# Performance work log

Measured on AMD Instinct MI355X. Metric: run time of the kernel, lower is better.

## Reference

```python
import jax, jax.numpy as jnp
import numpy as np

GAMMA = 2.0
ALPHA_CLASS = 0.01
ALPHA_COORD = 1.0

def _xywh_to_xyxy(b):
    # [.., 4] (x, y, w, h) -> (x1, y1, x2, y2)
    return jnp.concatenate([b[..., :2], b[..., :2] + b[..., 2:]], axis=-1)

def _jaccard(a, b):
    # a: [A,4] xyxy, b: [N,4] xyxy -> IoU [A,N]
    lt = jnp.maximum(a[:, None, :2], b[None, :, :2])
    rb = jnp.minimum(a[:, None, 2:], b[None, :, 2:])
    wh = jnp.clip(rb - lt, 0.0)
    inter = wh[..., 0] * wh[..., 1]
    area_a = (a[:, 2] - a[:, 0]) * (a[:, 3] - a[:, 1])
    area_b = (b[:, 2] - b[:, 0]) * (b[:, 3] - b[:, 1])
    return inter / (area_a[:, None] + area_b[None, :] - inter)

def _match_mask(thr, anchors, gt_xywh, num_obj):
    # Returns positive (anchor, gt) pair mask [A, N_max], honoring gt[:num_obj].
    A = anchors.shape[0]
    N = gt_xywh.shape[0]
    gt_boxes = _xywh_to_xyxy(gt_xywh)
    ious = _jaccard(anchors, gt_boxes)              # [A, N]
    valid = jnp.arange(N) < num_obj                 # [N]
    ious_v = jnp.where(valid[None, :], ious, -jnp.inf)
    best_gt_idx = jnp.argmax(ious_v, axis=0)        # [N] best anchor per gt
    forced = jnp.arange(A)[:, None] == best_gt_idx[None, :]  # positive_mask[best,i]=1
    return ((ious > thr) | forced) & valid[None, :]

def _class_loss_item(thr, classes, anchors, gt, num_obj):
    # classes: [A,2] probs (col0 = background, col1 = face)
    mask = _match_mask(thr, anchors, gt, num_obj)   # [A, N]
    counts = jnp.sum(mask, axis=1)                  # [A] multiplicity of each anchor in positive_idx
    is_pos = counts > 0                             # dedup, as index_fill_ does
    probs = jnp.where(is_pos, classes[:, 1], classes[:, 0])
    focal = -((1.0 - probs) ** GAMMA) * jnp.log(probs)
    # extra = focal_loss.index_select(0, positive_idx) keeps duplicates -> weight by counts
    extra = jnp.sum(counts.astype(focal.dtype) * focal)
    return jnp.sum(focal) + 10.0 * extra

def setup_inputs() -> dict:
    key = jax.random.key(0)
    B, A, N = 16, 131072, 64
    k1, k2, k3, k4, k5, k6 = jax.random.split(key, 6)
    # anchors in xyxy, valid boxes in [0,1]
    a_xy = jax.random.uniform(k1, (A, 2), jnp.float32, 0.0, 0.8)
    a_wh = jax.random.uniform(k2, (A, 2), jnp.float32, 0.05, 0.2)
    anchors = jnp.concatenate([a_xy, a_xy + a_wh], axis=-1)
    # class probabilities strictly in (0,1) for log()
    batch_classes = jax.random.uniform(k3, (B, A, 2), jnp.float32, 0.05, 0.95)
    g_xy = jax.random.uniform(k4, (B, N, 2), jnp.float32, 0.0, 0.8)
    g_wh = jax.random.uniform(k5, (B, N, 2), jnp.float32, 0.05, 0.2)
    batch_gt = jnp.concatenate([g_xy, g_wh], axis=-1)  # xywh
    batch_num_objects = jax.random.randint(k6, (B,), 1, N + 1, jnp.int32)
    return {
        "threshhold": jnp.float32(0.5),
        "batch_classes": batch_classes,
        "anchors": anchors,
        "batch_gt": batch_gt,
        "batch_num_objects": batch_num_objects,
    }

def reference(threshhold, batch_classes, anchors, batch_gt, batch_num_objects):
    R = batch_classes.shape[0]
    per_item = jax.vmap(lambda c, g, n: _class_loss_item(threshhold, c, anchors, g, n))
    class_loss = jnp.sum(per_item(batch_classes, batch_gt, batch_num_objects))
    class_loss = class_loss * ALPHA_CLASS / R
    # Faithful to the source: coord_loss is initialized to zero and never accumulated
    coord_loss = jnp.zeros((), batch_classes.dtype) * ALPHA_COORD / R
    total_loss = class_loss + coord_loss
    return (total_loss, class_loss, coord_loss)
```

## Files before the change

kernel.cpp:

```cpp
#include <hip/hip_runtime.h>

#define NANCH   131072
#define NMAX    64
#define NBATCH  16
#define THREADS 256
#define APT     4
#define ACH     (THREADS * APT)
#define NCHUNK  (NANCH / ACH)
#define NPAIR   (NBATCH / 2)
#define NBLK    (NCHUNK * NPAIR)
#define GTG     8


__global__ __launch_bounds__(64) void k_setup(
    const int* __restrict__ nobj, unsigned long long* __restrict__ cells,
    int* __restrict__ pairs)
{
    int tid = threadIdx.x;
    for (int i = tid; i < NBATCH * NMAX; i += 64) cells[i] = 0ull;
    if (tid == 0) {
        int idx[NBATCH], key[NBATCH];
        for (int i = 0; i < NBATCH; ++i) { idx[i] = i; key[i] = nobj[i]; }
        for (int i = 1; i < NBATCH; ++i) {
            int kj = key[i], ij = idx[i], j = i - 1;
            while (j >= 0 && key[j] < kj) { key[j+1]=key[j]; idx[j+1]=idx[j]; --j; }
            key[j+1] = kj; idx[j+1] = ij;
        }
        for (int p = 0; p < NPAIR; ++p) {
            pairs[2*p]   = idx[p];
            pairs[2*p+1] = idx[NBATCH-1-p];
        }
    }
}

__global__ __launch_bounds__(THREADS) void k_phase(
    const float* __restrict__ thr_p,
    const float* __restrict__ classes,
    const float* __restrict__ anchors,
    const float* __restrict__ gt,
    const int*   __restrict__ nobj,
    const int*   __restrict__ pairs,
    unsigned long long* __restrict__ cells,
    double* __restrict__ partials)
{
    int chunk = blockIdx.x / NPAIR;
    int pr    = blockIdx.x % NPAIR;
    int tid   = threadIdx.x;
    float thr = *thr_p;
    float t1  = 1.0f + thr;
    int b0 = pairs[2*pr], b1 = pairs[2*pr+1];

    __shared__ float4 sbox[2*NMAX];
    __shared__ float  sgar[2*NMAX];
    __shared__ float  stsg[2*NMAX];
    __shared__ int    sno[2];
    __shared__ unsigned long long spk[4][GTG];
    __shared__ double sw[4];

    for (int j = tid; j < 2*NMAX; j += THREADS) {
        int s = j >> 6, n = j & 63;
        int b = s ? b1 : b0;
        int no = nobj[b];
        float4 g = reinterpret_cast<const float4*>(gt)[b*NMAX + n];
        float x2 = g.x + g.z, y2 = g.y + g.w;
        float4 box = make_float4(g.x, g.y, x2, y2);
        float  ar  = (x2 - g.x) * (y2 - g.y);
        if (n >= no) { box = make_float4(4.f,4.f,4.f,4.f); ar = 0.f; }
        sbox[j] = box; sgar[j] = ar; stsg[j] = thr * ar;
    }
    if (tid < 2) sno[tid] = nobj[tid ? b1 : b0];
    __syncthreads();

    float ax1[APT], ay1[APT], ax2[APT], ay2[APT], aar[APT], ta[APT];
    int abase = chunk * ACH + tid;
    #pragma unroll
    for (int k = 0; k < APT; ++k) {
        float4 v = reinterpret_cast<const float4*>(anchors)[abase + k*THREADS];
        ax1[k]=v.x; ay1[k]=v.y; ax2[k]=v.z; ay2[k]=v.w;
        aar[k] = (v.z - v.x) * (v.w - v.y);
        ta[k]  = thr * aar[k];
    }

    int wv = tid >> 6, ln = tid & 63;
    double acc = 0.0;

    for (int s = 0; s < 2; ++s) {
        int b    = s ? b1 : b0;
        int no   = sno[s];
        int base = s * NMAX;
        int cnt[APT] = {0,0,0,0};

        for (int g0 = 0; g0 < no; g0 += GTG) {
            float bn[GTG], bd[GTG]; int bx[GTG];
            #pragma unroll
            for (int n = 0; n < GTG; ++n) { bn[n] = -1.f; bd[n] = 1.f; bx[n] = 0; }

            #pragma unroll
            for (int n = 0; n < GTG; ++n) {
                float4 g  = sbox[base + g0 + n];
                float gar = sgar[base + g0 + n];
                float tsg = stsg[base + g0 + n];
                #pragma unroll
                for (int k = 0; k < APT; ++k) {
                    float lx = fmaxf(ax1[k], g.x);
                    float ly = fmaxf(ay1[k], g.y);
                    float rx = fminf(ax2[k], g.z);
                    float ry = fminf(ay2[k], g.w);
                    float w  = fmaxf(rx - lx, 0.f);
                    float h  = fmaxf(ry - ly, 0.f);
                    float inter = w * h;
                    float den   = (aar[k] + gar) - inter;
                    cnt[k] += (inter * t1 > ta[k] + tsg) ? 1 : 0;
                    bool better = inter * bd[n] > bn[n] * den;
                    bn[n] = better ? inter : bn[n];
                    bd[n] = better ? den   : bd[n];
                    bx[n] = better ? (abase + k*THREADS) : bx[n];
                }
            }

            unsigned long long pk[GTG];
            #pragma unroll
            for (int n = 0; n < GTG; ++n) {
                float iou = bn[n] * __builtin_amdgcn_rcpf(bd[n]);
                pk[n] = ((unsigned long long)__float_as_uint(iou) << 32)
                      | (unsigned long long)(0x7FFFFFFFu - (unsigned)bx[n]);
            }
            #pragma unroll
            for (int off = 32; off; off >>= 1) {
                #pragma unroll
                for (int n = 0; n < GTG; ++n) {
                    unsigned long long o = __shfl_xor(pk[n], off, 64);
                    if (o > pk[n]) pk[n] = o;
                }
            }
            if (ln == 0) {
                #pragma unroll
                for (int n = 0; n < GTG; ++n) spk[wv][n] = pk[n];
            }
            __syncthreads();
            if (tid < GTG && g0 + tid < no) {
                unsigned long long m0 = spk[0][tid] > spk[1][tid] ? spk[0][tid] : spk[1][tid];
                unsigned long long m1 = spk[2][tid] > spk[3][tid] ? spk[2][tid] : spk[3][tid];
                unsigned long long m  = m0 > m1 ? m0 : m1;
                atomicMax(&cells[b*NMAX + g0 + tid], m);
            }
            __syncthreads();
        }

        const float2* cp = reinterpret_cast<const float2*>(classes) + (size_t)b * NANCH;
        #pragma unroll
        for (int k = 0; k < APT; ++k) {
            float2 c = cp[abase + k*THREADS];
            float p  = (cnt[k] > 0) ? c.y : c.x;
            float om = 1.0f - p;
            float focal = -om * om * __logf(p);
            acc += (double)(focal * (1.0f + 10.0f * (float)cnt[k]));
        }
    }

    #pragma unroll
    for (int off = 32; off; off >>= 1) acc += __shfl_xor(acc, off, 64);
    if (ln == 0) sw[wv] = acc;
    __syncthreads();
    if (tid == 0) partials[blockIdx.x] = sw[0] + sw[1] + sw[2] + sw[3];
}

__global__ __launch_bounds__(1024) void k_tail(
    const float* __restrict__ thr_p,
    const float* __restrict__ classes,
    const float* __restrict__ anchors,
    const float* __restrict__ gt,
    const int*   __restrict__ nobj,
    const unsigned long long* __restrict__ cells,
    const double* __restrict__ partials,
    float* __restrict__ out)
{
    int tid = threadIdx.x;
    int b = tid >> 6, n = tid & 63;
    float thr = *thr_p;
    float t1  = 1.0f + thr;

    __shared__ float4 sbox[NBATCH*NMAX];
    __shared__ float  stsa[NBATCH*NMAX];
    __shared__ int    sidx[NBATCH*NMAX];
    __shared__ double sdelta[NBATCH];
    __shared__ double sw[16];

    int n_obj = nobj[b];
    {
        float4 g = reinterpret_cast<const float4*>(gt)[b*NMAX + n];
        float x2 = g.x + g.z, y2 = g.y + g.w;
        sbox[tid] = make_float4(g.x, g.y, x2, y2);
        stsa[tid] = thr * ((x2 - g.x) * (y2 - g.y));
    }
    __syncthreads();

    int bi = -1; bool need = false;
    float4 av = make_float4(0.f,0.f,0.f,0.f);
    float ta = 0.f;
    if (n < n_obj) {
        unsigned long long pkv = cells[tid];
        bi = (int)(0x7FFFFFFFu - (unsigned)(pkv & 0xFFFFFFFFull));
        av = reinterpret_cast<const float4*>(anchors)[bi];
        float aar = (av.z - av.x) * (av.w - av.y);
        ta = thr * aar;
        float4 g = sbox[tid];
        float lx = fmaxf(av.x, g.x), ly = fmaxf(av.y, g.y);
        float rx = fminf(av.z, g.z), ry = fminf(av.w, g.w);
        float w  = fmaxf(rx - lx, 0.f), h = fmaxf(ry - ly, 0.f);
        float inter = w * h;
        need = !(inter * t1 > ta + stsa[tid]);
    }
    sidx[tid] = need ? bi : -1;
    __syncthreads();

    double delta = 0.0;
    if (need) {
        bool first = true; int extra = 0;
        int base = b * NMAX;
        for (int m = 0; m < NMAX; ++m) {
            if (sidx[base + m] == bi) { if (m < n) first = false; ++extra; }
        }
        if (first) {
            int count = 0;
            for (int m = 0; m < n_obj; ++m) {
                float4 g = sbox[base + m];
                float lx = fmaxf(av.x, g.x), ly = fmaxf(av.y, g.y);
                float rx = fminf(av.z, g.z), ry = fminf(av.w, g.w);
                float w  = fmaxf(rx - lx, 0.f), h = fmaxf(ry - ly, 0.f);
                float inter = w * h;
                count += (inter * t1 > ta + stsa[base + m]) ? 1 : 0;
            }
            float2 c = reinterpret_cast<const float2*>(classes)[(size_t)b * NANCH + bi];
            float po = (count > 0) ? c.y : c.x;
            float oo = 1.f - po;
            float fo = -oo * oo * __logf(po);
            float oldc = fo * (1.f + 10.f * (float)count);
            int cn = count + extra;
            float pn = (cn > 0) ? c.y : c.x;
            float on = 1.f - pn;
            float fn = -on * on * __logf(pn);
            float newc = fn * (1.f + 10.f * (float)cn);
            delta = (double)newc - (double)oldc;
        }
    }
    #pragma unroll
    for (int off = 32; off; off >>= 1) delta += __shfl_xor(delta, off, 64);
    if (n == 0) sdelta[b] = delta;
    __syncthreads();

    double v = partials[tid];
    if (tid < NBATCH) v += sdelta[tid];
    #pragma unroll
    for (int off = 32; off; off >>= 1) v += __shfl_xor(v, off, 64);
    if ((tid & 63) == 0) sw[tid >> 6] = v;
    __syncthreads();
    if (tid == 0) {
        double tot = 0.0;
        #pragma unroll
        for (int i = 0; i < 16; ++i) tot += sw[i];
        double cls = tot * (0.01 / 16.0);
        out[0] = (float)cls;
        out[1] = (float)cls;
        out[2] = 0.0f;
    }
}

extern "C" void kernel_launch(void* const* d_in, const int* in_sizes, int n_in,
                              void* d_out, int out_size, void* d_ws, size_t ws_size,
                              hipStream_t stream) {
    const float* thr     = (const float*)d_in[0];
    const float* classes = (const float*)d_in[1];
    const float* anchors = (const float*)d_in[2];
    const float* gt      = (const float*)d_in[3];
    const int*   nobj    = (const int*)d_in[4];
    float* out = (float*)d_out;

    unsigned long long* cells = (unsigned long long*)d_ws;
    int*    pairs    = (int*)((char*)d_ws + NBATCH * NMAX * sizeof(unsigned long long));
    double* partials = (double*)((char*)d_ws + NBATCH * NMAX * sizeof(unsigned long long) + 64);

    k_setup<<<1, 64, 0, stream>>>(nobj, cells, pairs);
    k_phase<<<NBLK, THREADS, 0, stream>>>(thr, classes, anchors, gt, nobj, pairs,
                                          cells, partials);
    k_tail<<<1, 1024, 0, stream>>>(thr, classes, anchors, gt, nobj, cells, partials, out);
}
```

Before: 91.29 us.

## Halve block size, double anchors per thread, and drop block-level argmax reduction

```diff
diff --git a/kernel.cpp b/kernel.cpp
--- a/kernel.cpp
+++ b/kernel.cpp
@@ -3,8 +3,8 @@
 #define NANCH   131072
 #define NMAX    64
 #define NBATCH  16
-#define THREADS 256
-#define APT     4
+#define THREADS 128
+#define APT     8
 #define ACH     (THREADS * APT)
 #define NCHUNK  (NANCH / ACH)
 #define NPAIR   (NBATCH / 2)
@@ -47,38 +47,34 @@
     int pr    = blockIdx.x % NPAIR;
     int tid   = threadIdx.x;
     float thr = *thr_p;
-    float t1  = 1.0f + thr;
     int b0 = pairs[2*pr], b1 = pairs[2*pr+1];
+    int no0 = nobj[b0], no1 = nobj[b1];
 
     __shared__ float4 sbox[2*NMAX];
     __shared__ float  sgar[2*NMAX];
-    __shared__ float  stsg[2*NMAX];
-    __shared__ int    sno[2];
-    __shared__ unsigned long long spk[4][GTG];
-    __shared__ double sw[4];
-
-    for (int j = tid; j < 2*NMAX; j += THREADS) {
+    {
+        int j = tid;
         int s = j >> 6, n = j & 63;
-        int b = s ? b1 : b0;
-        int no = nobj[b];
+        int b  = s ? b1 : b0;
+        int no = s ? no1 : no0;
         float4 g = reinterpret_cast<const float4*>(gt)[b*NMAX + n];
         float x2 = g.x + g.z, y2 = g.y + g.w;
         float4 box = make_float4(g.x, g.y, x2, y2);
         float  ar  = (x2 - g.x) * (y2 - g.y);
         if (n >= no) { box = make_float4(4.f,4.f,4.f,4.f); ar = 0.f; }
-        sbox[j] = box; sgar[j] = ar; stsg[j] = thr * ar;
-    }
-    if (tid < 2) sno[tid] = nobj[tid ? b1 : b0];
-    __syncthreads();
-
-    float ax1[APT], ay1[APT], ax2[APT], ay2[APT], aar[APT], ta[APT];
+        sbox[j] = box; sgar[j] = ar;
+    }
+    __syncthreads();
+
+    float ax1[APT], ay1[APT], ax2[APT], ay2[APT], aar[APT];
+    int   aidx[APT];
     int abase = chunk * ACH + tid;
     #pragma unroll
     for (int k = 0; k < APT; ++k) {
-        float4 v = reinterpret_cast<const float4*>(anchors)[abase + k*THREADS];
+        aidx[k] = abase + k * THREADS;
+        float4 v = reinterpret_cast<const float4*>(anchors)[aidx[k]];
         ax1[k]=v.x; ay1[k]=v.y; ax2[k]=v.z; ay2[k]=v.w;
         aar[k] = (v.z - v.x) * (v.w - v.y);
-        ta[k]  = thr * aar[k];
     }
 
     int wv = tid >> 6, ln = tid & 63;
@@ -86,9 +82,11 @@
 
     for (int s = 0; s < 2; ++s) {
         int b    = s ? b1 : b0;
-        int no   = sno[s];
+        int no   = s ? no1 : no0;
         int base = s * NMAX;
-        int cnt[APT] = {0,0,0,0};
+        int cnt[APT];
+        #pragma unroll
+        for (int k = 0; k < APT; ++k) cnt[k] = 0;
 
         for (int g0 = 0; g0 < no; g0 += GTG) {
             float bn[GTG], bd[GTG]; int bx[GTG];
@@ -99,7 +97,6 @@
             for (int n = 0; n < GTG; ++n) {
                 float4 g  = sbox[base + g0 + n];
                 float gar = sgar[base + g0 + n];
-                float tsg = stsg[base + g0 + n];
                 #pragma unroll
                 for (int k = 0; k < APT; ++k) {
                     float lx = fmaxf(ax1[k], g.x);
@@ -110,11 +107,11 @@
                     float h  = fmaxf(ry - ly, 0.f);
                     float inter = w * h;
                     float den   = (aar[k] + gar) - inter;
-                    cnt[k] += (inter * t1 > ta[k] + tsg) ? 1 : 0;
+                    cnt[k] += (inter > thr * den) ? 1 : 0;
                     bool better = inter * bd[n] > bn[n] * den;
-                    bn[n] = better ? inter : bn[n];
-                    bd[n] = better ? den   : bd[n];
-                    bx[n] = better ? (abase + k*THREADS) : bx[n];
+                    bn[n] = better ? inter   : bn[n];
+                    bd[n] = better ? den     : bd[n];
+                    bx[n] = better ? aidx[k] : bx[n];
                 }
             }
 
@@ -135,22 +132,15 @@
             }
             if (ln == 0) {
                 #pragma unroll
-                for (int n = 0; n < GTG; ++n) spk[wv][n] = pk[n];
-            }
-            __syncthreads();
-            if (tid < GTG && g0 + tid < no) {
-                unsigned long long m0 = spk[0][tid] > spk[1][tid] ? spk[0][tid] : spk[1][tid];
-                unsigned long long m1 = spk[2][tid] > spk[3][tid] ? spk[2][tid] : spk[3][tid];
-                unsigned long long m  = m0 > m1 ? m0 : m1;
-                atomicMax(&cells[b*NMAX + g0 + tid], m);
-            }
-            __syncthreads();
+                for (int n = 0; n < GTG; ++n)
+                    if (g0 + n < no) atomicMax(&cells[b*NMAX + g0 + n], pk[n]);
+            }
         }
 
         const float2* cp = reinterpret_cast<const float2*>(classes) + (size_t)b * NANCH;
         #pragma unroll
         for (int k = 0; k < APT; ++k) {
-            float2 c = cp[abase + k*THREADS];
+            float2 c = cp[aidx[k]];
             float p  = (cnt[k] > 0) ? c.y : c.x;
             float om = 1.0f - p;
             float focal = -om * om * __logf(p);
@@ -160,9 +150,10 @@
 
     #pragma unroll
     for (int off = 32; off; off >>= 1) acc += __shfl_xor(acc, off, 64);
+    __shared__ double sw[2];
     if (ln == 0) sw[wv] = acc;
     __syncthreads();
-    if (tid == 0) partials[blockIdx.x] = sw[0] + sw[1] + sw[2] + sw[3];
+    if (tid == 0) partials[blockIdx.x] = sw[0] + sw[1];
 }
 
 __global__ __launch_bounds__(1024) void k_tail(
@@ -178,10 +169,9 @@
     int tid = threadIdx.x;
     int b = tid >> 6, n = tid & 63;
     float thr = *thr_p;
-    float t1  = 1.0f + thr;
 
     __shared__ float4 sbox[NBATCH*NMAX];
-    __shared__ float  stsa[NBATCH*NMAX];
+    __shared__ float  sar[NBATCH*NMAX];
     __shared__ int    sidx[NBATCH*NMAX];
     __shared__ double sdelta[NBATCH];
     __shared__ double sw[16];
@@ -191,25 +181,25 @@
         float4 g = reinterpret_cast<const float4*>(gt)[b*NMAX + n];
         float x2 = g.x + g.z, y2 = g.y + g.w;
         sbox[tid] = make_float4(g.x, g.y, x2, y2);
-        stsa[tid] = thr * ((x2 - g.x) * (y2 - g.y));
+        sar[tid]  = (x2 - g.x) * (y2 - g.y);
     }
     __syncthreads();
 
     int bi = -1; bool need = false;
     float4 av = make_float4(0.f,0.f,0.f,0.f);
-    float ta = 0.f;
+    float aar = 0.f;
     if (n < n_obj) {
         unsigned long long pkv = cells[tid];
         bi = (int)(0x7FFFFFFFu - (unsigned)(pkv & 0xFFFFFFFFull));
         av = reinterpret_cast<const float4*>(anchors)[bi];
-        float aar = (av.z - av.x) * (av.w - av.y);
-        ta = thr * aar;
+        aar = (av.z - av.x) * (av.w - av.y);
         float4 g = sbox[tid];
         float lx = fmaxf(av.x, g.x), ly = fmaxf(av.y, g.y);
         float rx = fminf(av.z, g.z), ry = fminf(av.w, g.w);
         float w  = fmaxf(rx - lx, 0.f), h = fmaxf(ry - ly, 0.f);
         float inter = w * h;
-        need = !(inter * t1 > ta + stsa[tid]);
+        float den   = (aar + sar[tid]) - inter;
+        need = !(inter > thr * den);
     }
     sidx[tid] = need ? bi : -1;
     __syncthreads();
@@ -229,7 +219,8 @@
                 float rx = fminf(av.z, g.z), ry = fminf(av.w, g.w);
                 float w  = fmaxf(rx - lx, 0.f), h = fmaxf(ry - ly, 0.f);
                 float inter = w * h;
-                count += (inter * t1 > ta + stsa[base + m]) ? 1 : 0;
+                float den   = (aar + sar[base + m]) - inter;
+                count += (inter > thr * den) ? 1 : 0;
             }
             float2 c = reinterpret_cast<const float2*>(classes)[(size_t)b * NANCH + bi];
             float po = (count > 0) ? c.y : c.x;
```

Result: slower. 134.5 us (+47.4%).
